# Kernel tuning notes

Measured on AMD Instinct MI355X. Metric: run time of the kernel, lower is better.

The kernel has to match this reference:

```python
import jax, jax.numpy as jnp
import numpy as np

B, D_IN, D_FEAT = 256, 512, 512   # batch, encoder in-dim, encoder out-dim (= Sender input_dim)
H, V, E, L = 512, 32000, 64, 16   # hidden_size, vocab_size, embedding_dim, length


def setup_inputs() -> dict:
    key = jax.random.key(0)
    ks = jax.random.split(key, 12)
    s = lambda *d: 1.0 / np.sqrt(d[-1])
    return {
        "x": jax.random.normal(ks[0], (B, D_IN), jnp.float32),
        # encoder: Linear(D_IN, D_FEAT)
        "enc_W": jax.random.normal(ks[1], (D_FEAT, D_IN), jnp.float32) * s(D_IN),
        "enc_b": jnp.zeros((D_FEAT,), jnp.float32),
        # input_layer: Linear(D_FEAT, H)
        "in_W": jax.random.normal(ks[2], (H, D_FEAT), jnp.float32) * s(D_FEAT),
        "in_b": jnp.zeros((H,), jnp.float32),
        # GRU cell (torch layout: gates ordered r, z, n)
        "W_ih": jax.random.normal(ks[3], (3 * H, E), jnp.float32) * s(H),
        "W_hh": jax.random.normal(ks[4], (3 * H, H), jnp.float32) * s(H),
        "b_ih": jnp.zeros((3 * H,), jnp.float32),
        "b_hh": jnp.zeros((3 * H,), jnp.float32),
        # output_layer: Linear(H, V)
        "out_W": jax.random.normal(ks[5], (V, H), jnp.float32) * s(H),
        "out_b": jnp.zeros((V,), jnp.float32),
        # msg_embedding table and sos embedding parameter
        "emb_table": jax.random.normal(ks[6], (V, E), jnp.float32),
        "sos_emb": jax.random.normal(ks[7], (E,), jnp.float32),
    }


def _gru_cell(e, h, W_ih, W_hh, b_ih, b_hh):
    gi = e @ W_ih.T + b_ih            # [B, 3H]
    gh = h @ W_hh.T + b_hh            # [B, 3H]
    gi_r, gi_z, gi_n = jnp.split(gi, 3, axis=-1)
    gh_r, gh_z, gh_n = jnp.split(gh, 3, axis=-1)
    r = jax.nn.sigmoid(gi_r + gh_r)
    z = jax.nn.sigmoid(gi_z + gh_z)
    n = jnp.tanh(gi_n + r * gh_n)
    return (1.0 - z) * n + z * h


def reference(x, enc_W, enc_b, in_W, in_b, W_ih, W_hh, b_ih, b_hh,
              out_W, out_b, emb_table, sos_emb):
    # encoder -> input_layer -> initial hidden state (num_layers = 1)
    feat = x @ enc_W.T + enc_b                  # [B, D_FEAT]
    h0 = feat @ in_W.T + in_b                   # [B, H]
    e0 = jnp.broadcast_to(sos_emb, (x.shape[0], E))  # sos embedding repeated over batch

    def step(carry, _):
        h, e = carry
        h = _gru_cell(e, h, W_ih, W_hh, b_ih, b_hh)      # [B, H]
        logits_t = h @ out_W.T + out_b                    # [B, V]
        sym = jnp.argmax(logits_t, axis=-1)               # eval-mode greedy symbol [B]
        e_next = emb_table[sym]                           # [B, E]
        return (h, e_next), (sym, logits_t)

    (_, _), (syms, logits) = jax.lax.scan(step, (h0, e0), None, length=L)
    sequence = syms.T                                     # [B, L] int
    logits = jnp.transpose(logits, (1, 0, 2))             # [B, L, V]
    return sequence, logits
```

## Files before the change

kernel.cpp:

```cpp
#include <hip/hip_runtime.h>
#include <math.h>

#define BATCH 256
#define DIN 512
#define DFEAT 512
#define HSZ 512
#define VOCAB 32000
#define EMB 64
#define SLEN 16
#define NTILE 500
#define MARGIN 0.0625f

typedef __attribute__((ext_vector_type(8))) short bf16x8;
typedef __attribute__((ext_vector_type(4))) float f32x4;

__device__ inline unsigned bf16_rne(float x) {
    union { float f; unsigned u; } u; u.f = x;
    unsigned r = u.u + 0x7fff + ((u.u >> 16) & 1);
    return r >> 16;
}

template<int BM, int BN, int BK, int TM, int TN>
__global__ __launch_bounds__(256) void gemm_atb(
    const float* __restrict__ A,
    const float* __restrict__ W,
    const float* __restrict__ bias,
    float* __restrict__ C, long long ldc,
    int M, int N, int K)
{
    __shared__ float As[BK][BM + 4];
    __shared__ float Bs[BK][BN + 4];
    constexpr int THREADS = (BM / TM) * (BN / TN);
    const int tid = threadIdx.x;
    const int tx = tid % (BN / TN);
    const int ty = tid / (BN / TN);
    const int row0 = blockIdx.y * BM;
    const int col0 = blockIdx.x * BN;
    float acc[TM][TN] = {};
    for (int k0 = 0; k0 < K; k0 += BK) {
        for (int i = tid; i < BM * BK; i += THREADS) {
            int m = i / BK, k = i % BK;
            As[k][m] = A[(long long)(row0 + m) * K + k0 + k];
        }
        for (int i = tid; i < BN * BK; i += THREADS) {
            int n = i / BK, k = i % BK;
            Bs[k][n] = W[(long long)(col0 + n) * K + k0 + k];
        }
        __syncthreads();
        #pragma unroll
        for (int kk = 0; kk < BK; ++kk) {
            float a[TM], b[TN];
            #pragma unroll
            for (int i = 0; i < TM; ++i) a[i] = As[kk][ty * TM + i];
            #pragma unroll
            for (int j = 0; j < TN; ++j) b[j] = Bs[kk][tx * TN + j];
            #pragma unroll
            for (int i = 0; i < TM; ++i)
                #pragma unroll
                for (int j = 0; j < TN; ++j)
                    acc[i][j] = fmaf(a[i], b[j], acc[i][j]);
        }
        __syncthreads();
    }
    #pragma unroll
    for (int i = 0; i < TM; ++i) {
        long long m = row0 + ty * TM + i;
        float* crow = C + m * ldc;
        #pragma unroll
        for (int j = 0; j < TN; ++j) {
            int n = col0 + tx * TN + j;
            float v = acc[i][j];
            if (bias) v += bias[n];
            crow[n] = v;
        }
    }
}

__global__ void prep_kernel(const float* __restrict__ out_W, ushort* __restrict__ Wb,
                            const float* __restrict__ W_ih, const float* __restrict__ W_hh,
                            const float* __restrict__ b_ih, const float* __restrict__ b_hh,
                            float* __restrict__ Wcat2, float* __restrict__ bcat2,
                            int* __restrict__ done)
{
    const int stride = gridDim.x * 256;
    const int t0 = blockIdx.x * 256 + threadIdx.x;
    for (int i = t0; i < VOCAB * HSZ / 4; i += stride) {
        const float4 v = ((const float4*)out_W)[i];
        ushort4 o;
        o.x = (ushort)bf16_rne(v.x); o.y = (ushort)bf16_rne(v.y);
        o.z = (ushort)bf16_rne(v.z); o.w = (ushort)bf16_rne(v.w);
        ((ushort4*)Wb)[i] = o;
    }
    for (long long i = t0; i < 2048LL * 576; i += stride) {
        int g = (int)(i / 576), k = (int)(i % 576);
        int j = g >> 2, comp = g & 3;
        float v;
        if (comp == 0)      v = (k < 64) ? W_ih[j * 64 + k]          : W_hh[(long long)j * 512 + k - 64];
        else if (comp == 1) v = (k < 64) ? W_ih[(512 + j) * 64 + k]  : W_hh[(long long)(512 + j) * 512 + k - 64];
        else if (comp == 2) v = (k < 64) ? W_ih[(1024 + j) * 64 + k] : 0.f;
        else                v = (k < 64) ? 0.f                        : W_hh[(long long)(1024 + j) * 512 + k - 64];
        Wcat2[i] = v;
    }
    for (int i = t0; i < 2048; i += stride) {
        int j = i >> 2, comp = i & 3;
        float bv = (comp == 0) ? b_ih[j] + b_hh[j]
                 : (comp == 1) ? b_ih[512 + j] + b_hh[512 + j]
                 : (comp == 2) ? b_ih[1024 + j] : b_hh[1024 + j];
        bcat2[i] = bv;
    }
    if (t0 == 0) { done[0] = 0; done[8] = 0; }
}


__device__ __forceinline__ int argmax_body(int b, int tprev,
    const float* __restrict__ tmaxv, const float* __restrict__ lprev,
    const float* __restrict__ hprev, const float* __restrict__ out_W,
    const float* __restrict__ out_b, float* __restrict__ seq, char* sm)
{
    float* s_red = (float*)sm;
    int*   s_qt  = (int*)(sm + 1024);
    int*   s_cand= (int*)(sm + 1280);
    float* s_rv  = (float*)(sm + 1536);
    int*   s_cnt = (int*)(sm + 1792);
    int*   s_sym = (int*)(sm + 1800);
    const int tid = threadIdx.x;
    const int lane = tid & 63, wave = tid >> 6;
    const float* row = lprev + (long long)b * (SLEN * (long long)VOCAB);

    float v0 = tmaxv[(long long)b * 512 + tid];
    float v1 = (tid + 256 < NTILE) ? tmaxv[(long long)b * 512 + 256 + tid] : -INFINITY;
    s_red[tid] = fmaxf(v0, v1); __syncthreads();
    for (int s = 128; s > 0; s >>= 1) {
        if (tid < s) s_red[tid] = fmaxf(s_red[tid], s_red[tid + s]);
        __syncthreads();
    }
    float M = s_red[0];
    if (tid == 0) { s_cnt[0] = 0; s_cnt[1] = 0; }
    __syncthreads();
    if (v0 >= M - MARGIN) {
        int s = atomicAdd(&s_cnt[0], 1);
        if (s < 64) s_qt[s] = tid;
    }
    if (v1 >= M - MARGIN) {
        int s = atomicAdd(&s_cnt[0], 1);
        if (s < 64) s_qt[s] = tid + 256;
    }
    __syncthreads();
    int nq = min(s_cnt[0], 64);
    for (int idx = tid; idx < nq * 64; idx += 256) {
        int c = s_qt[idx >> 6] * 64 + (idx & 63);
        if (row[c] >= M - MARGIN) {
            int s = atomicAdd(&s_cnt[1], 1);
            if (s < 64) s_cand[s] = c;
        }
    }
    __syncthreads();
    int nc = min(s_cnt[1], 64);
    const float* hrow = hprev + (long long)b * 512;
    for (int ci = wave; ci < nc; ci += 4) {
        int vv = s_cand[ci];
        const float* wrow = out_W + (long long)vv * 512;
        float s = 0.f;
        for (int k = lane; k < 512; k += 64) s = fmaf(hrow[k], wrow[k], s);
        for (int off = 32; off > 0; off >>= 1) s += __shfl_down(s, off, 64);
        if (lane == 0) s_rv[ci] = s + out_b[vv];
    }
    __syncthreads();
    if (tid == 0) {
        float bv = -INFINITY; int sym = 0x7fffffff;
        for (int ci = 0; ci < nc; ++ci) {
            float xx = s_rv[ci]; int c = s_cand[ci];
            if (xx > bv || (xx == bv && c < sym)) { bv = xx; sym = c; }
        }
        if (sym < 0 || sym >= VOCAB) sym = 0;
        seq[b * SLEN + tprev] = (float)sym;
        *s_sym = sym;
    }
    __syncthreads();
    return *s_sym;
}

__device__ __forceinline__ void logits_body(int bid,
    const ushort* __restrict__ hbf, const ushort* __restrict__ Wb,
    const float* __restrict__ out_b, float* __restrict__ lbase,
    float* __restrict__ tmaxv, char* sm)
{
    char* As = sm;
    char* Bs = sm + 16384;
    float* s_mv = (float*)(sm + 24576);
    const int tid = threadIdx.x;
    const int lane = tid & 63;
    const int wave = tid >> 6;
    const int job = (bid & 7) * 125 + (bid >> 3);
    const int jx = job >> 1;
    const int jy = job & 1;
    const int row0 = jy * 128;
    const int col0 = jx * 64;

    f32x4 acc[2][4] = {};
    const int srow = tid >> 3;
    const int sch = tid & 7;

    for (int k0 = 0; k0 < 512; k0 += 64) {
        #pragma unroll
        for (int ra = 0; ra < 4; ++ra) {
            int row = ra * 32 + srow;
            const char* g = (const char*)(hbf + (long long)(row0 + row) * 512 + k0) + ((sch ^ (row & 7)) * 16);
            __builtin_amdgcn_global_load_lds(
                (const __attribute__((address_space(1))) void*)g,
                (__attribute__((address_space(3))) void*)(As + row * 128 + sch * 16), 16, 0, 0);
        }
        #pragma unroll
        for (int rb = 0; rb < 2; ++rb) {
            int row = rb * 32 + srow;
            const char* g = (const char*)(Wb + (long long)(col0 + row) * 512 + k0) + ((sch ^ (row & 7)) * 16);
            __builtin_amdgcn_global_load_lds(
                (const __attribute__((address_space(1))) void*)g,
                (__attribute__((address_space(3))) void*)(Bs + row * 128 + sch * 16), 16, 0, 0);
        }
        __syncthreads();
        #pragma unroll
        for (int k32 = 0; k32 < 64; k32 += 32) {
            bf16x8 af[2], bfr[4];
            #pragma unroll
            for (int f = 0; f < 2; ++f) {
                int rA = wave * 32 + f * 16 + (lane & 15);
                int byteA = (rA * 128 + (k32 + ((lane >> 4) << 3)) * 2) ^ ((rA & 7) << 4);
                af[f] = *(const bf16x8*)&As[byteA];
            }
            #pragma unroll
            for (int j = 0; j < 4; ++j) {
                int rB = j * 16 + (lane & 15);
                int byteB = (rB * 128 + (k32 + ((lane >> 4) << 3)) * 2) ^ ((rB & 7) << 4);
                bfr[j] = *(const bf16x8*)&Bs[byteB];
            }
            #pragma unroll
            for (int f = 0; f < 2; ++f)
                #pragma unroll
                for (int j = 0; j < 4; ++j)
                    acc[f][j] = __builtin_amdgcn_mfma_f32_16x16x32_bf16(af[f], bfr[j], acc[f][j], 0, 0, 0);
        }
        __syncthreads();
    }

    #pragma unroll
    for (int f = 0; f < 2; ++f) {
        #pragma unroll
        for (int q = 0; q < 4; ++q) {
            int r_local = wave * 32 + f * 16 + ((lane >> 4) << 2) + q;
            float* crow = lbase + (long long)(row0 + r_local) * (SLEN * (long long)VOCAB);
            float mv = -INFINITY;
            #pragma unroll
            for (int j = 0; j < 4; ++j) {
                int c = col0 + j * 16 + (lane & 15);
                float v = acc[f][j][q] + out_b[c];
                __builtin_nontemporal_store(v, &crow[c]);
                mv = fmaxf(mv, v);
            }
            #pragma unroll
            for (int m = 1; m < 16; m <<= 1) mv = fmaxf(mv, __shfl_xor(mv, m, 64));
            if ((lane & 15) == 0) s_mv[r_local] = mv;
        }
    }
    __syncthreads();
    if (tid < 128)
        tmaxv[(long long)(row0 + tid) * 512 + jx] = s_mv[tid];
}

template<bool FIRST, bool MERGED>
__device__ __forceinline__ void gru_body(int blk,
    const float* __restrict__ hprev, float* __restrict__ hnew,
    const float* __restrict__ Wcat2, const float* __restrict__ bcat2,
    float* __restrict__ ebuf, const float* __restrict__ sos,
    unsigned* __restrict__ hbfu, int* __restrict__ done, int wt_e, char* sm)
{
    const int tid = threadIdx.x;
    const int ty = blk >> 5;
    const int tx = blk & 31;
    float* As = (float*)sm;
    float* Bs = (float*)(sm + 4608);
    const int tyt = tid >> 4;
    const int txt = tid & 15;
    float acc[4] = {};

    for (int k0 = 64; k0 < 576; k0 += 64) {
        for (int i = tid; i < 16 * 64; i += 256) {
            int m = i >> 6, k = i & 63;
            As[k * 18 + m] = hprev[(long long)(ty * 16 + m) * 512 + (k0 - 64) + k];
        }
        for (int i = tid; i < 64 * 64; i += 256) {
            int n = i >> 6, k = i & 63;
            Bs[k * 68 + n] = Wcat2[(long long)(tx * 64 + n) * 576 + k0 + k];
        }
        __syncthreads();
        #pragma unroll 8
        for (int kk = 0; kk < 64; ++kk) {
            const float a = As[kk * 18 + tyt];
            const float4 b = *(const float4*)&Bs[kk * 68 + txt * 4];
            acc[0] = fmaf(a, b.x, acc[0]);
            acc[1] = fmaf(a, b.y, acc[1]);
            acc[2] = fmaf(a, b.z, acc[2]);
            acc[3] = fmaf(a, b.w, acc[3]);
        }
        __syncthreads();
    }

    if (!FIRST) {
        if (tid == 0) {
            while (__hip_atomic_load(&done[0], __ATOMIC_RELAXED, __HIP_MEMORY_SCOPE_AGENT) < wt_e)
                __builtin_amdgcn_s_sleep(8);
            __hip_atomic_load(&done[0], __ATOMIC_ACQUIRE, __HIP_MEMORY_SCOPE_AGENT);
        }
        __syncthreads();
    }
    {
        for (int i = tid; i < 16 * 64; i += 256) {
            int m = i >> 6, k = i & 63;
            float v;
            if (FIRST) v = sos[k];
            else v = __hip_atomic_load(&ebuf[(long long)(ty * 16 + m) * EMB + k],
                                       __ATOMIC_RELAXED, __HIP_MEMORY_SCOPE_AGENT);
            As[k * 18 + m] = v;
        }
        for (int i = tid; i < 64 * 64; i += 256) {
            int n = i >> 6, k = i & 63;
            Bs[k * 68 + n] = Wcat2[(long long)(tx * 64 + n) * 576 + k];
        }
        __syncthreads();
        #pragma unroll 8
        for (int kk = 0; kk < 64; ++kk) {
            const float a = As[kk * 18 + tyt];
            const float4 b = *(const float4*)&Bs[kk * 68 + txt * 4];
            acc[0] = fmaf(a, b.x, acc[0]);
            acc[1] = fmaf(a, b.y, acc[1]);
            acc[2] = fmaf(a, b.z, acc[2]);
            acc[3] = fmaf(a, b.w, acc[3]);
        }
        __syncthreads();
    }

    float* gt = (float*)sm;
    ushort* sh_hb = (ushort*)(sm + 8192);
    #pragma unroll
    for (int j = 0; j < 4; ++j)
        gt[tyt * 64 + txt * 4 + j] = acc[j];
    __syncthreads();
    {
        int row = tid >> 4, jl = tid & 15;
        int jg = tx * 16 + jl;
        float gr  = gt[row * 64 + jl * 4 + 0] + bcat2[jg * 4 + 0];
        float gz  = gt[row * 64 + jl * 4 + 1] + bcat2[jg * 4 + 1];
        float gni = gt[row * 64 + jl * 4 + 2] + bcat2[jg * 4 + 2];
        float gnh = gt[row * 64 + jl * 4 + 3] + bcat2[jg * 4 + 3];
        float r = 1.0f / (1.0f + expf(-gr));
        float z = 1.0f / (1.0f + expf(-gz));
        float n = tanhf(gni + r * gnh);
        long long bglob = ty * 16 + row;
        float hold = hprev[bglob * 512 + jg];
        float h = (1.0f - z) * n + z * hold;
        hnew[bglob * 512 + jg] = h;
        sh_hb[row * 16 + jl] = (ushort)bf16_rne(h);
    }
    __syncthreads();
    if (tid < 128) {
        int row = tid >> 3, jp = tid & 7;
        unsigned lo = sh_hb[row * 16 + jp * 2];
        unsigned hi = sh_hb[row * 16 + jp * 2 + 1];
        unsigned v = (hi << 16) | lo;
        long long idx = (long long)(ty * 16 + row) * 256 + tx * 8 + jp;
        if (MERGED)
            __hip_atomic_store(&hbfu[idx], v, __ATOMIC_RELAXED, __HIP_MEMORY_SCOPE_AGENT);
        else
            hbfu[idx] = v;
    }
    if (MERGED) {
        __syncthreads();
        if (tid == 0)
            __hip_atomic_fetch_add(&done[8], 1, __ATOMIC_RELEASE, __HIP_MEMORY_SCOPE_AGENT);
    }
}

template<bool FIRST>
__global__ __launch_bounds__(256) void gl_kernel(
    const float* __restrict__ hprev, float* __restrict__ hnew,
    const float* __restrict__ Wcat2, const float* __restrict__ bcat2,
    float* __restrict__ ebuf, const float* __restrict__ sos,
    unsigned* __restrict__ hbfu, const ushort* __restrict__ Wb,
    const float* __restrict__ out_W, const float* __restrict__ out_b,
    const float* __restrict__ emb, float* __restrict__ seq,
    float* __restrict__ tmaxv, const float* __restrict__ lprev,
    float* __restrict__ lbase, int* __restrict__ done,
    int wt_e, int wt_l, int tprev)
{
    __shared__ __align__(16) char smem[25600];
    const int tid = threadIdx.x;
    const int bid = blockIdx.x;

    if (!FIRST && bid < BATCH) {
        int sym = argmax_body(bid, tprev, tmaxv, lprev, hprev, out_W, out_b, seq, smem);
        if (tid < EMB)
            __hip_atomic_store(&ebuf[(long long)bid * EMB + tid],
                               emb[(long long)sym * EMB + tid],
                               __ATOMIC_RELAXED, __HIP_MEMORY_SCOPE_AGENT);
        __syncthreads();
        if (tid == 0)
            __hip_atomic_fetch_add(&done[0], 1, __ATOMIC_RELEASE, __HIP_MEMORY_SCOPE_AGENT);
        __syncthreads();
    }

    if (bid < 512)
        gru_body<FIRST, true>(bid, hprev, hnew, Wcat2, bcat2, ebuf, sos, hbfu, done, wt_e, smem);

    if (tid == 0) {
        while (__hip_atomic_load(&done[8], __ATOMIC_RELAXED, __HIP_MEMORY_SCOPE_AGENT) < wt_l)
            __builtin_amdgcn_s_sleep(8);
        __hip_atomic_load(&done[8], __ATOMIC_ACQUIRE, __HIP_MEMORY_SCOPE_AGENT);
    }
    __syncthreads();
    logits_body(bid, (const ushort*)hbfu, Wb, out_b, lbase, tmaxv, smem);
}

template<bool FIRST>
__global__ __launch_bounds__(256) void ag2_kernel(
    const float* __restrict__ hprev, float* __restrict__ hnew,
    const float* __restrict__ Wcat2, const float* __restrict__ bcat2,
    float* __restrict__ ebuf, const float* __restrict__ sos,
    unsigned* __restrict__ hbfu,
    const float* __restrict__ tmaxv, const float* __restrict__ lprev,
    const float* __restrict__ out_W, const float* __restrict__ out_b,
    const float* __restrict__ emb, float* __restrict__ seq,
    int* __restrict__ done, int wt_e, int tprev)
{
    __shared__ __align__(16) char smem[25600];
    const int tid = threadIdx.x;
    const int bid = blockIdx.x;
    if (!FIRST && bid < BATCH) {
        int sym = argmax_body(bid, tprev, tmaxv, lprev, hprev, out_W, out_b, seq, smem);
        if (tid < EMB)
            __hip_atomic_store(&ebuf[(long long)bid * EMB + tid],
                               emb[(long long)sym * EMB + tid],
                               __ATOMIC_RELAXED, __HIP_MEMORY_SCOPE_AGENT);
        __syncthreads();
        if (tid == 0)
            __hip_atomic_fetch_add(&done[0], 1, __ATOMIC_RELEASE, __HIP_MEMORY_SCOPE_AGENT);
        __syncthreads();
    }
    gru_body<FIRST, false>(bid, hprev, hnew, Wcat2, bcat2, ebuf, sos, hbfu, done, wt_e, smem);
}

__global__ __launch_bounds__(256) void logits_bm128_kernel(
    const ushort* __restrict__ hbf, const ushort* __restrict__ Wb,
    const float* __restrict__ out_b,
    float* __restrict__ lbase, float* __restrict__ tmaxv)
{
    __shared__ __align__(16) char smem[25600];
    logits_body(blockIdx.x, hbf, Wb, out_b, lbase, tmaxv, smem);
}

__global__ __launch_bounds__(256) void argmax_final(
    const float* __restrict__ tmaxv, const float* __restrict__ lbase,
    const float* __restrict__ h, const float* __restrict__ out_W,
    const float* __restrict__ out_b, float* __restrict__ seq, int t)
{
    __shared__ __align__(16) char smem[2048];
    argmax_body(blockIdx.x, t, tmaxv, lbase, h, out_W, out_b, seq, smem);
}

extern "C" void kernel_launch(void* const* d_in, const int* in_sizes, int n_in,
                              void* d_out, int out_size, void* d_ws, size_t ws_size,
                              hipStream_t stream) {
    const float* x     = (const float*)d_in[0];
    const float* enc_W = (const float*)d_in[1];
    const float* enc_b = (const float*)d_in[2];
    const float* in_W  = (const float*)d_in[3];
    const float* in_b  = (const float*)d_in[4];
    const float* W_ih  = (const float*)d_in[5];
    const float* W_hh  = (const float*)d_in[6];
    const float* b_ih  = (const float*)d_in[7];
    const float* b_hh  = (const float*)d_in[8];
    const float* out_W = (const float*)d_in[9];
    const float* out_b = (const float*)d_in[10];
    const float* emb   = (const float*)d_in[11];
    const float* sos   = (const float*)d_in[12];

    float* seq    = (float*)d_out;
    float* logits = (float*)d_out + BATCH * SLEN;

    char* p = (char*)d_ws;
    ushort* Wb    = (ushort*)p;  p += (size_t)VOCAB * HSZ * 2;
    float* Wcat2  = (float*)p;   p += (size_t)2048 * 576 * 4;
    float* bcat2  = (float*)p;   p += 2048 * 4;
    float* hA     = (float*)p;   p += (size_t)BATCH * HSZ * 4;
    float* hB     = (float*)p;   p += (size_t)BATCH * HSZ * 4;
    unsigned* hbfu= (unsigned*)p; p += (size_t)BATCH * HSZ * 2;
    float* ebuf   = (float*)p;   p += (size_t)BATCH * EMB * 4;
    float* feat   = (float*)p;   p += (size_t)BATCH * DFEAT * 4;
    float* tmaxv  = (float*)p;   p += (size_t)BATCH * 512 * 4;
    int*   done   = (int*)p;     p += 64;

    prep_kernel<<<1024, 256, 0, stream>>>(out_W, Wb, W_ih, W_hh, b_ih, b_hh,
                                          Wcat2, bcat2, done);
    gemm_atb<64, 64, 32, 4, 4><<<dim3(DFEAT / 64, BATCH / 64), 256, 0, stream>>>(
        x, enc_W, enc_b, feat, DFEAT, BATCH, DFEAT, DIN);
    gemm_atb<64, 64, 32, 4, 4><<<dim3(HSZ / 64, BATCH / 64), 256, 0, stream>>>(
        feat, in_W, in_b, hA, HSZ, BATCH, HSZ, DFEAT);

    int nb = 0;
    hipError_t qerr = hipOccupancyMaxActiveBlocksPerMultiprocessor(
        &nb, reinterpret_cast<const void*>(gl_kernel<false>), 256, 0);
    bool merged = (qerr == hipSuccess && nb >= 4);

    float* hc = hA;
    float* hn = hB;
    for (int t = 0; t < SLEN; ++t) {
        float* lbase = logits + (long long)t * VOCAB;
        const float* lprev = logits + (long long)(t > 0 ? t - 1 : 0) * VOCAB;
        if (merged) {
            if (t == 0) {
                gl_kernel<true><<<1000, 256, 0, stream>>>(
                    hc, hn, Wcat2, bcat2, ebuf, sos, hbfu, Wb, out_W, out_b, emb, seq,
                    tmaxv, lprev, lbase, done, 0, 512, 0);
            } else {
                gl_kernel<false><<<1000, 256, 0, stream>>>(
                    hc, hn, Wcat2, bcat2, ebuf, sos, hbfu, Wb, out_W, out_b, emb, seq,
                    tmaxv, lprev, lbase, done, 256 * t, 512 * (t + 1), t - 1);
            }
        } else {
            if (t == 0) {
                ag2_kernel<true><<<512, 256, 0, stream>>>(
                    hc, hn, Wcat2, bcat2, ebuf, sos, hbfu,
                    tmaxv, lprev, out_W, out_b, emb, seq, done, 0, 0);
            } else {
                ag2_kernel<false><<<512, 256, 0, stream>>>(
                    hc, hn, Wcat2, bcat2, ebuf, sos, hbfu,
                    tmaxv, lprev, out_W, out_b, emb, seq, done, 256 * t, t - 1);
            }
            logits_bm128_kernel<<<1000, 256, 0, stream>>>(
                (const ushort*)hbfu, Wb, out_b, lbase, tmaxv);
        }
        float* tmp = hc; hc = hn; hn = tmp;
    }
    argmax_final<<<BATCH, 256, 0, stream>>>(
        tmaxv, logits + (long long)(SLEN - 1) * VOCAB, hc, out_W, out_b, seq, SLEN - 1);
}
```

Baseline: 1.155 ms.

## Fuse all decode steps into one persistent kernel with per-step flag counters

Replaces the per-timestep launches of the merged GRU+logits kernel with a single persistent 1000-block kernel that loops over all 16 steps. Steps are ordered by fine-grained per-step atomic counters, split per batch half, instead of kernel boundaries. Hidden state, bf16 hidden, embedding input and tile-max buffers are now kept per step so no step overwrites data another block still reads. This removes launch gaps and lets argmax, GRU and logits overlap across halves of the batch. In exchange it uses much more workspace, relies on all 1000 blocks being co-resident, and spin-waits with relaxed atomic stores on the logits.

```diff
diff --git a/kernel.cpp b/kernel.cpp
--- a/kernel.cpp
+++ b/kernel.cpp
@@ -20,12 +20,18 @@
     return r >> 16;
 }
 
+__device__ inline void poll_ge(int* c, int target) {
+    while (__hip_atomic_load(c, __ATOMIC_RELAXED, __HIP_MEMORY_SCOPE_AGENT) < target)
+        __builtin_amdgcn_s_sleep(8);
+}
+__device__ inline void bump(int* c) {
+    __hip_atomic_fetch_add(c, 1, __ATOMIC_RELEASE, __HIP_MEMORY_SCOPE_AGENT);
+}
+
 template<int BM, int BN, int BK, int TM, int TN>
 __global__ __launch_bounds__(256) void gemm_atb(
-    const float* __restrict__ A,
-    const float* __restrict__ W,
-    const float* __restrict__ bias,
-    float* __restrict__ C, long long ldc,
+    const float* __restrict__ A, const float* __restrict__ W,
+    const float* __restrict__ bias, float* __restrict__ C, long long ldc,
     int M, int N, int K)
 {
     __shared__ float As[BK][BM + 4];
@@ -108,13 +114,13 @@
                  : (comp == 2) ? b_ih[1024 + j] : b_hh[1024 + j];
         bcat2[i] = bv;
     }
-    if (t0 == 0) { done[0] = 0; done[8] = 0; }
+    for (int i = t0; i < 256; i += stride) done[i] = 0;
 }
 
 
 __device__ __forceinline__ int argmax_body(int b, int tprev,
     const float* __restrict__ tmaxv, const float* __restrict__ lprev,
-    const float* __restrict__ hprev, const float* __restrict__ out_W,
+    const float* __restrict__ href, const float* __restrict__ out_W,
     const float* __restrict__ out_b, float* __restrict__ seq, char* sm)
 {
     float* s_red = (float*)sm;
@@ -137,14 +143,8 @@
     float M = s_red[0];
     if (tid == 0) { s_cnt[0] = 0; s_cnt[1] = 0; }
     __syncthreads();
-    if (v0 >= M - MARGIN) {
-        int s = atomicAdd(&s_cnt[0], 1);
-        if (s < 64) s_qt[s] = tid;
-    }
-    if (v1 >= M - MARGIN) {
-        int s = atomicAdd(&s_cnt[0], 1);
-        if (s < 64) s_qt[s] = tid + 256;
-    }
+    if (v0 >= M - MARGIN) { int s = atomicAdd(&s_cnt[0], 1); if (s < 64) s_qt[s] = tid; }
+    if (v1 >= M - MARGIN) { int s = atomicAdd(&s_cnt[0], 1); if (s < 64) s_qt[s] = tid + 256; }
     __syncthreads();
     int nq = min(s_cnt[0], 64);
     for (int idx = tid; idx < nq * 64; idx += 256) {
@@ -156,7 +156,7 @@
     }
     __syncthreads();
     int nc = min(s_cnt[1], 64);
-    const float* hrow = hprev + (long long)b * 512;
+    const float* hrow = href + (long long)b * 512;
     for (int ci = wave; ci < nc; ci += 4) {
         int vv = s_cand[ci];
         const float* wrow = out_W + (long long)vv * 512;
@@ -180,95 +180,8 @@
     return *s_sym;
 }
 
-__device__ __forceinline__ void logits_body(int bid,
-    const ushort* __restrict__ hbf, const ushort* __restrict__ Wb,
-    const float* __restrict__ out_b, float* __restrict__ lbase,
-    float* __restrict__ tmaxv, char* sm)
-{
-    char* As = sm;
-    char* Bs = sm + 16384;
-    float* s_mv = (float*)(sm + 24576);
-    const int tid = threadIdx.x;
-    const int lane = tid & 63;
-    const int wave = tid >> 6;
-    const int job = (bid & 7) * 125 + (bid >> 3);
-    const int jx = job >> 1;
-    const int jy = job & 1;
-    const int row0 = jy * 128;
-    const int col0 = jx * 64;
-
-    f32x4 acc[2][4] = {};
-    const int srow = tid >> 3;
-    const int sch = tid & 7;
-
-    for (int k0 = 0; k0 < 512; k0 += 64) {
-        #pragma unroll
-        for (int ra = 0; ra < 4; ++ra) {
-            int row = ra * 32 + srow;
-            const char* g = (const char*)(hbf + (long long)(row0 + row) * 512 + k0) + ((sch ^ (row & 7)) * 16);
-            __builtin_amdgcn_global_load_lds(
-                (const __attribute__((address_space(1))) void*)g,
-                (__attribute__((address_space(3))) void*)(As + row * 128 + sch * 16), 16, 0, 0);
-        }
-        #pragma unroll
-        for (int rb = 0; rb < 2; ++rb) {
-            int row = rb * 32 + srow;
-            const char* g = (const char*)(Wb + (long long)(col0 + row) * 512 + k0) + ((sch ^ (row & 7)) * 16);
-            __builtin_amdgcn_global_load_lds(
-                (const __attribute__((address_space(1))) void*)g,
-                (__attribute__((address_space(3))) void*)(Bs + row * 128 + sch * 16), 16, 0, 0);
-        }
-        __syncthreads();
-        #pragma unroll
-        for (int k32 = 0; k32 < 64; k32 += 32) {
-            bf16x8 af[2], bfr[4];
-            #pragma unroll
-            for (int f = 0; f < 2; ++f) {
-                int rA = wave * 32 + f * 16 + (lane & 15);
-                int byteA = (rA * 128 + (k32 + ((lane >> 4) << 3)) * 2) ^ ((rA & 7) << 4);
-                af[f] = *(const bf16x8*)&As[byteA];
-            }
-            #pragma unroll
-            for (int j = 0; j < 4; ++j) {
-                int rB = j * 16 + (lane & 15);
-                int byteB = (rB * 128 + (k32 + ((lane >> 4) << 3)) * 2) ^ ((rB & 7) << 4);
-                bfr[j] = *(const bf16x8*)&Bs[byteB];
-            }
-            #pragma unroll
-            for (int f = 0; f < 2; ++f)
-                #pragma unroll
-                for (int j = 0; j < 4; ++j)
-                    acc[f][j] = __builtin_amdgcn_mfma_f32_16x16x32_bf16(af[f], bfr[j], acc[f][j], 0, 0, 0);
-        }
-        __syncthreads();
-    }
-
-    #pragma unroll
-    for (int f = 0; f < 2; ++f) {
-        #pragma unroll
-        for (int q = 0; q < 4; ++q) {
-            int r_local = wave * 32 + f * 16 + ((lane >> 4) << 2) + q;
-            float* crow = lbase + (long long)(row0 + r_local) * (SLEN * (long long)VOCAB);
-            float mv = -INFINITY;
-            #pragma unroll
-            for (int j = 0; j < 4; ++j) {
-                int c = col0 + j * 16 + (lane & 15);
-                float v = acc[f][j][q] + out_b[c];
-                __builtin_nontemporal_store(v, &crow[c]);
-                mv = fmaxf(mv, v);
-            }
-            #pragma unroll
-            for (int m = 1; m < 16; m <<= 1) mv = fmaxf(mv, __shfl_xor(mv, m, 64));
-            if ((lane & 15) == 0) s_mv[r_local] = mv;
-        }
-    }
-    __syncthreads();
-    if (tid < 128)
-        tmaxv[(long long)(row0 + tid) * 512 + jx] = s_mv[tid];
-}
-
-template<bool FIRST, bool MERGED>
-__device__ __forceinline__ void gru_body(int blk,
+template<bool FIRST, bool PERSIST>
+__device__ __forceinline__ void gru_body(int blk, int t,
     const float* __restrict__ hprev, float* __restrict__ hnew,
     const float* __restrict__ Wcat2, const float* __restrict__ bcat2,
     float* __restrict__ ebuf, const float* __restrict__ sos,
@@ -283,6 +196,10 @@
     const int txt = tid & 15;
     float acc[4] = {};
 
+    if (PERSIST && !FIRST) {
+        if (tid == 0) poll_ge(done + (t - 1) * 8 + 1 + (ty >= 8 ? 1 : 0), 256);
+        __syncthreads();
+    }
     for (int k0 = 64; k0 < 576; k0 += 64) {
         for (int i = tid; i < 16 * 64; i += 256) {
             int m = i >> 6, k = i & 63;
@@ -306,11 +223,7 @@
     }
 
     if (!FIRST) {
-        if (tid == 0) {
-            while (__hip_atomic_load(&done[0], __ATOMIC_RELAXED, __HIP_MEMORY_SCOPE_AGENT) < wt_e)
-                __builtin_amdgcn_s_sleep(8);
-            __hip_atomic_load(&done[0], __ATOMIC_ACQUIRE, __HIP_MEMORY_SCOPE_AGENT);
-        }
+        if (tid == 0) poll_ge(done + (PERSIST ? t * 8 + 0 : 0), wt_e);
         __syncthreads();
     }
     {
@@ -318,8 +231,7 @@
             int m = i >> 6, k = i & 63;
             float v;
             if (FIRST) v = sos[k];
-            else v = __hip_atomic_load(&ebuf[(long long)(ty * 16 + m) * EMB + k],
-                                       __ATOMIC_RELAXED, __HIP_MEMORY_SCOPE_AGENT);
+            else v = ebuf[(long long)(ty * 16 + m) * EMB + k];
             As[k * 18 + m] = v;
         }
         for (int i = tid; i < 64 * 64; i += 256) {
@@ -358,7 +270,11 @@
         long long bglob = ty * 16 + row;
         float hold = hprev[bglob * 512 + jg];
         float h = (1.0f - z) * n + z * hold;
-        hnew[bglob * 512 + jg] = h;
+        if (PERSIST)
+            __hip_atomic_store(&hnew[bglob * 512 + jg], h,
+                               __ATOMIC_RELAXED, __HIP_MEMORY_SCOPE_AGENT);
+        else
+            hnew[bglob * 512 + jg] = h;
         sh_hb[row * 16 + jl] = (ushort)bf16_rne(h);
     }
     __syncthreads();
@@ -368,56 +284,182 @@
         unsigned hi = sh_hb[row * 16 + jp * 2 + 1];
         unsigned v = (hi << 16) | lo;
         long long idx = (long long)(ty * 16 + row) * 256 + tx * 8 + jp;
-        if (MERGED)
+        if (PERSIST)
             __hip_atomic_store(&hbfu[idx], v, __ATOMIC_RELAXED, __HIP_MEMORY_SCOPE_AGENT);
         else
             hbfu[idx] = v;
     }
-    if (MERGED) {
-        __syncthreads();
-        if (tid == 0)
-            __hip_atomic_fetch_add(&done[8], 1, __ATOMIC_RELEASE, __HIP_MEMORY_SCOPE_AGENT);
-    }
-}
-
-template<bool FIRST>
-__global__ __launch_bounds__(256) void gl_kernel(
-    const float* __restrict__ hprev, float* __restrict__ hnew,
+    if (PERSIST) {
+        __syncthreads();
+        if (tid == 0) bump(done + t * 8 + 1 + (ty >= 8 ? 1 : 0));
+    }
+}
+
+template<bool PERSIST>
+__device__ __forceinline__ void logits_body(int bid, int t,
+    const ushort* __restrict__ hbf, const ushort* __restrict__ Wb,
+    const float* __restrict__ out_b, float* __restrict__ lbase,
+    float* __restrict__ tmaxv, int* __restrict__ done, char* sm)
+{
+    char* As = sm;
+    char* Bs = sm + 16384;
+    float* s_mv = (float*)(sm + 24576);
+    const int tid = threadIdx.x;
+    const int lane = tid & 63;
+    const int wave = tid >> 6;
+    const int job = (bid & 7) * 125 + (bid >> 3);
+    const int jx = job >> 1;
+    const int jy = job & 1;
+    const int row0 = jy * 128;
+    const int col0 = jx * 64;
+
+    if (PERSIST) {
+        if (tid == 0) poll_ge(done + t * 8 + 1 + jy, 256);
+        __syncthreads();
+    }
+
+    f32x4 acc[2][4] = {};
+    const int srow = tid >> 3;
+    const int sch = tid & 7;
+
+    for (int k0 = 0; k0 < 512; k0 += 64) {
+        #pragma unroll
+        for (int ra = 0; ra < 4; ++ra) {
+            int row = ra * 32 + srow;
+            const char* g = (const char*)(hbf + (long long)(row0 + row) * 512 + k0) + ((sch ^ (row & 7)) * 16);
+            __builtin_amdgcn_global_load_lds(
+                (const __attribute__((address_space(1))) void*)g,
+                (__attribute__((address_space(3))) void*)(As + row * 128 + sch * 16), 16, 0, 0);
+        }
+        #pragma unroll
+        for (int rb = 0; rb < 2; ++rb) {
+            int row = rb * 32 + srow;
+            const char* g = (const char*)(Wb + (long long)(col0 + row) * 512 + k0) + ((sch ^ (row & 7)) * 16);
+            __builtin_amdgcn_global_load_lds(
+                (const __attribute__((address_space(1))) void*)g,
+                (__attribute__((address_space(3))) void*)(Bs + row * 128 + sch * 16), 16, 0, 0);
+        }
+        __syncthreads();
+        #pragma unroll
+        for (int k32 = 0; k32 < 64; k32 += 32) {
+            bf16x8 af[2], bfr[4];
+            #pragma unroll
+            for (int f = 0; f < 2; ++f) {
+                int rA = wave * 32 + f * 16 + (lane & 15);
+                int byteA = (rA * 128 + (k32 + ((lane >> 4) << 3)) * 2) ^ ((rA & 7) << 4);
+                af[f] = *(const bf16x8*)&As[byteA];
+            }
+            #pragma unroll
+            for (int j = 0; j < 4; ++j) {
+                int rB = j * 16 + (lane & 15);
+                int byteB = (rB * 128 + (k32 + ((lane >> 4) << 3)) * 2) ^ ((rB & 7) << 4);
+                bfr[j] = *(const bf16x8*)&Bs[byteB];
+            }
+            #pragma unroll
+            for (int f = 0; f < 2; ++f)
+                #pragma unroll
+                for (int j = 0; j < 4; ++j)
+                    acc[f][j] = __builtin_amdgcn_mfma_f32_16x16x32_bf16(af[f], bfr[j], acc[f][j], 0, 0, 0);
+        }
+        __syncthreads();
+    }
+
+    #pragma unroll
+    for (int f = 0; f < 2; ++f) {
+        #pragma unroll
+        for (int q = 0; q < 4; ++q) {
+            int r_local = wave * 32 + f * 16 + ((lane >> 4) << 2) + q;
+            float* crow = lbase + (long long)(row0 + r_local) * (SLEN * (long long)VOCAB);
+            float mv = -INFINITY;
+            #pragma unroll
+            for (int j = 0; j < 4; ++j) {
+                int c = col0 + j * 16 + (lane & 15);
+                float v = acc[f][j][q] + out_b[c];
+                if (PERSIST)
+                    __hip_atomic_store(&crow[c], v, __ATOMIC_RELAXED, __HIP_MEMORY_SCOPE_AGENT);
+                else
+                    __builtin_nontemporal_store(v, &crow[c]);
+                mv = fmaxf(mv, v);
+            }
+            #pragma unroll
+            for (int m = 1; m < 16; m <<= 1) mv = fmaxf(mv, __shfl_xor(mv, m, 64));
+            if ((lane & 15) == 0) s_mv[r_local] = mv;
+        }
+    }
+    __syncthreads();
+    if (tid < 128) {
+        float v = s_mv[tid];
+        if (PERSIST)
+            __hip_atomic_store(&tmaxv[(long long)(row0 + tid) * 512 + jx], v,
+                               __ATOMIC_RELAXED, __HIP_MEMORY_SCOPE_AGENT);
+        else
+            tmaxv[(long long)(row0 + tid) * 512 + jx] = v;
+    }
+    if (PERSIST) {
+        __syncthreads();
+        if (tid == 0) bump(done + t * 8 + 3 + jy);
+    }
+}
+
+__global__ __launch_bounds__(256) void persist_kernel(
+    float* __restrict__ hbase,
     const float* __restrict__ Wcat2, const float* __restrict__ bcat2,
-    float* __restrict__ ebuf, const float* __restrict__ sos,
-    unsigned* __restrict__ hbfu, const ushort* __restrict__ Wb,
+    float* __restrict__ ebase,
+    const float* __restrict__ sos,
+    unsigned* __restrict__ hbase_u,
+    const ushort* __restrict__ Wb,
     const float* __restrict__ out_W, const float* __restrict__ out_b,
     const float* __restrict__ emb, float* __restrict__ seq,
-    float* __restrict__ tmaxv, const float* __restrict__ lprev,
-    float* __restrict__ lbase, int* __restrict__ done,
-    int wt_e, int wt_l, int tprev)
+    float* __restrict__ tmbase,
+    float* __restrict__ logits,
+    int* __restrict__ done)
 {
     __shared__ __align__(16) char smem[25600];
     const int tid = threadIdx.x;
     const int bid = blockIdx.x;
 
-    if (!FIRST && bid < BATCH) {
-        int sym = argmax_body(bid, tprev, tmaxv, lprev, hprev, out_W, out_b, seq, smem);
-        if (tid < EMB)
-            __hip_atomic_store(&ebuf[(long long)bid * EMB + tid],
-                               emb[(long long)sym * EMB + tid],
-                               __ATOMIC_RELAXED, __HIP_MEMORY_SCOPE_AGENT);
-        __syncthreads();
-        if (tid == 0)
-            __hip_atomic_fetch_add(&done[0], 1, __ATOMIC_RELEASE, __HIP_MEMORY_SCOPE_AGENT);
-        __syncthreads();
-    }
-
-    if (bid < 512)
-        gru_body<FIRST, true>(bid, hprev, hnew, Wcat2, bcat2, ebuf, sos, hbfu, done, wt_e, smem);
-
-    if (tid == 0) {
-        while (__hip_atomic_load(&done[8], __ATOMIC_RELAXED, __HIP_MEMORY_SCOPE_AGENT) < wt_l)
-            __builtin_amdgcn_s_sleep(8);
-        __hip_atomic_load(&done[8], __ATOMIC_ACQUIRE, __HIP_MEMORY_SCOPE_AGENT);
-    }
-    __syncthreads();
-    logits_body(bid, (const ushort*)hbfu, Wb, out_b, lbase, tmaxv, smem);
+    for (int t = 0; t <= SLEN; ++t) {
+        if (t > 0 && bid < BATCH) {
+            const int half = (bid >= 128) ? 1 : 0;
+            if (tid == 0) poll_ge(done + (t - 1) * 8 + 3 + half, 500);
+            __syncthreads();
+            int sym = argmax_body(bid, t - 1,
+                                  tmbase + (long long)(t - 1) * BATCH * 512,
+                                  logits + (long long)(t - 1) * VOCAB,
+                                  hbase + (long long)t * BATCH * HSZ,
+                                  out_W, out_b, seq, smem);
+            if (t < SLEN) {
+                if (tid < EMB)
+                    __hip_atomic_store(&ebase[(long long)t * BATCH * EMB + (long long)bid * EMB + tid],
+                                       emb[(long long)sym * EMB + tid],
+                                       __ATOMIC_RELAXED, __HIP_MEMORY_SCOPE_AGENT);
+                __syncthreads();
+                if (tid == 0) bump(done + t * 8 + 0);
+            }
+            __syncthreads();
+        }
+        if (t == SLEN) break;
+
+        if (bid < 512) {
+            if (t == 0)
+                gru_body<true, true>(bid, t,
+                    hbase, hbase + (long long)BATCH * HSZ,
+                    Wcat2, bcat2, ebase, sos,
+                    hbase_u, done, 0, smem);
+            else
+                gru_body<false, true>(bid, t,
+                    hbase + (long long)t * BATCH * HSZ,
+                    hbase + (long long)(t + 1) * BATCH * HSZ,
+                    Wcat2, bcat2,
+                    ebase + (long long)t * BATCH * EMB, sos,
+                    hbase_u + (long long)t * BATCH * 256, done, 256, smem);
+        }
+
+        logits_body<true>(bid, t,
+            (const ushort*)(hbase_u + (long long)t * BATCH * 256), Wb, out_b,
+            logits + (long long)t * VOCAB,
+            tmbase + (long long)t * BATCH * 512, done, smem);
+    }
 }
 
 template<bool FIRST>
@@ -441,11 +483,10 @@
                                emb[(long long)sym * EMB + tid],
                                __ATOMIC_RELAXED, __HIP_MEMORY_SCOPE_AGENT);
         __syncthreads();
-        if (tid == 0)
-            __hip_atomic_fetch_add(&done[0], 1, __ATOMIC_RELEASE, __HIP_MEMORY_SCOPE_AGENT);
-        __syncthreads();
-    }
-    gru_body<FIRST, false>(bid, hprev, hnew, Wcat2, bcat2, ebuf, sos, hbfu, done, wt_e, smem);
+        if (tid == 0) bump(done);
+        __syncthreads();
+    }
+    gru_body<FIRST, false>(bid, 0, hprev, hnew, Wcat2, bcat2, ebuf, sos, hbfu, done, wt_e, smem);
 }
 
 __global__ __launch_bounds__(256) void logits_bm128_kernel(
@@ -454,7 +495,7 @@
     float* __restrict__ lbase, float* __restrict__ tmaxv)
 {
     __shared__ __align__(16) char smem[25600];
-    logits_body(blockIdx.x, hbf, Wb, out_b, lbase, tmaxv, smem);
+    logits_body<false>(blockIdx.x, 0, hbf, Wb, out_b, lbase, tmaxv, nullptr, smem);
 }
 
 __global__ __launch_bounds__(256) void argmax_final(
@@ -487,59 +528,74 @@
     float* logits = (float*)d_out + BATCH * SLEN;
 
     char* p = (char*)d_ws;
-    ushort* Wb    = (ushort*)p;  p += (size_t)VOCAB * HSZ * 2;
-    float* Wcat2  = (float*)p;   p += (size_t)2048 * 576 * 4;
-    float* bcat2  = (float*)p;   p += 2048 * 4;
-    float* hA     = (float*)p;   p += (size_t)BATCH * HSZ * 4;
-    float* hB     = (float*)p;   p += (size_t)BATCH * HSZ * 4;
-    unsigned* hbfu= (unsigned*)p; p += (size_t)BATCH * HSZ * 2;
-    float* ebuf   = (float*)p;   p += (size_t)BATCH * EMB * 4;
-    float* feat   = (float*)p;   p += (size_t)BATCH * DFEAT * 4;
-    float* tmaxv  = (float*)p;   p += (size_t)BATCH * 512 * 4;
-    int*   done   = (int*)p;     p += 64;
+    ushort* Wb    = (ushort*)p;   p += (size_t)VOCAB * HSZ * 2;
+    float* Wcat2  = (float*)p;    p += (size_t)2048 * 576 * 4;
+    float* bcat2  = (float*)p;    p += 2048 * 4;
+    float* feat   = (float*)p;    p += (size_t)BATCH * DFEAT * 4;
+    int*   done   = (int*)p;      p += 1024;
+    float* hbase  = (float*)p;    p += (size_t)2 * BATCH * HSZ * 4;
+    unsigned* hbu = (unsigned*)p; p += (size_t)BATCH * HSZ * 2;
+    float* ebase  = (float*)p;    p += (size_t)BATCH * EMB * 4;
+    float* tmbase = (float*)p;    p += (size_t)BATCH * 512 * 4;
+    size_t base_need = (size_t)(p - (char*)d_ws);
+
+    size_t persist_need = (size_t)VOCAB * HSZ * 2 + 2048LL * 576 * 4 + 2048 * 4
+        + (size_t)BATCH * DFEAT * 4 + 1024
+        + 17LL * BATCH * HSZ * 4
+        + 16LL * BATCH * HSZ * 2
+        + 16LL * BATCH * EMB * 4
+        + 16LL * BATCH * 512 * 4;
+
+    int nb = 0;
+    hipError_t qerr = hipOccupancyMaxActiveBlocksPerMultiprocessor(
+        &nb, reinterpret_cast<const void*>(persist_kernel), 256, 0);
+    bool persist = (qerr == hipSuccess) && (nb >= 4) && (ws_size >= persist_need);
+
+    if (persist) {
+        char* q = (char*)d_ws;
+        Wb    = (ushort*)q;   q += (size_t)VOCAB * HSZ * 2;
+        Wcat2 = (float*)q;    q += (size_t)2048 * 576 * 4;
+        bcat2 = (float*)q;    q += 2048 * 4;
+        feat  = (float*)q;    q += (size_t)BATCH * DFEAT * 4;
+        done  = (int*)q;      q += 1024;
+        hbase = (float*)q;    q += 17LL * BATCH * HSZ * 4;
+        hbu   = (unsigned*)q; q += 16LL * BATCH * HSZ * 2;
+        ebase = (float*)q;    q += 16LL * BATCH * EMB * 4;
+        tmbase= (float*)q;    q += 16LL * BATCH * 512 * 4;
+    }
+    (void)base_need;
 
     prep_kernel<<<1024, 256, 0, stream>>>(out_W, Wb, W_ih, W_hh, b_ih, b_hh,
                                           Wcat2, bcat2, done);
     gemm_atb<64, 64, 32, 4, 4><<<dim3(DFEAT / 64, BATCH / 64), 256, 0, stream>>>(
         x, enc_W, enc_b, feat, DFEAT, BATCH, DFEAT, DIN);
     gemm_atb<64, 64, 32, 4, 4><<<dim3(HSZ / 64, BATCH / 64), 256, 0, stream>>>(
-        feat, in_W, in_b, hA, HSZ, BATCH, HSZ, DFEAT);
-
-    int nb = 0;
-    hipError_t qerr = hipOccupancyMaxActiveBlocksPerMultiprocessor(
-        &nb, reinterpret_cast<const void*>(gl_kernel<false>), 256, 0);
-    bool merged = (qerr == hipSuccess && nb >= 4);
-
-    float* hc = hA;
-    float* hn = hB;
-    for (int t = 0; t < SLEN; ++t) {
-        float* lbase = logits + (long long)t * VOCAB;
-        const float* lprev = logits + (long long)(t > 0 ? t - 1 : 0) * VOCAB;
-        if (merged) {
-            if (t == 0) {
-                gl_kernel<true><<<1000, 256, 0, stream>>>(
-                    hc, hn, Wcat2, bcat2, ebuf, sos, hbfu, Wb, out_W, out_b, emb, seq,
-                    tmaxv, lprev, lbase, done, 0, 512, 0);
-            } else {
-                gl_kernel<false><<<1000, 256, 0, stream>>>(
-                    hc, hn, Wcat2, bcat2, ebuf, sos, hbfu, Wb, out_W, out_b, emb, seq,
-                    tmaxv, lprev, lbase, done, 256 * t, 512 * (t + 1), t - 1);
-            }
-        } else {
+        feat, in_W, in_b, hbase, HSZ, BATCH, HSZ, DFEAT);
+
+    if (persist) {
+        persist_kernel<<<1000, 256, 0, stream>>>(
+            hbase, Wcat2, bcat2, ebase, sos, hbu, Wb,
+            out_W, out_b, emb, seq, tmbase, logits, done);
+    } else {
+        float* hc = hbase;
+        float* hn = hbase + (size_t)BATCH * HSZ;
+        for (int t = 0; t < SLEN; ++t) {
+            float* lbase = logits + (long long)t * VOCAB;
+            const float* lprev = logits + (long long)(t > 0 ? t - 1 : 0) * VOCAB;
             if (t == 0) {
                 ag2_kernel<true><<<512, 256, 0, stream>>>(
-                    hc, hn, Wcat2, bcat2, ebuf, sos, hbfu,
-                    tmaxv, lprev, out_W, out_b, emb, seq, done, 0, 0);
+                    hc, hn, Wcat2, bcat2, ebase, sos, hbu,
+                    tmbase, lprev, out_W, out_b, emb, seq, done, 0, 0);
             } else {
                 ag2_kernel<false><<<512, 256, 0, stream>>>(
-                    hc, hn, Wcat2, bcat2, ebuf, sos, hbfu,
-                    tmaxv, lprev, out_W, out_b, emb, seq, done, 256 * t, t - 1);
+                    hc, hn, Wcat2, bcat2, ebase, sos, hbu,
+                    tmbase, lprev, out_W, out_b, emb, seq, done, 256 * t, t - 1);
             }
             logits_bm128_kernel<<<1000, 256, 0, stream>>>(
-                (const ushort*)hbfu, Wb, out_b, lbase, tmaxv);
-        }
-        float* tmp = hc; hc = hn; hn = tmp;
-    }
-    argmax_final<<<BATCH, 256, 0, stream>>>(
-        tmaxv, logits + (long long)(SLEN - 1) * VOCAB, hc, out_W, out_b, seq, SLEN - 1);
-}
+                (const ushort*)hbu, Wb, out_b, lbase, tmbase);
+            float* tmp = hc; hc = hn; hn = tmp;
+        }
+        argmax_final<<<BATCH, 256, 0, stream>>>(
+            tmbase, logits + (long long)(SLEN - 1) * VOCAB, hc, out_W, out_b, seq, SLEN - 1);
+    }
+}
```

Result: faster. 1.124 ms (-2.7%).
